# Kernel optimization log

Hardware: AMD Instinct MI355X
Metric: run time of the kernel (lower is better)

The kernel has to match this reference:

```python
import jax, jax.numpy as jnp
import numpy as np


def _pairwise_l2(x, y):
    # x: [N, D], y: [M, D] -> [N, M] Euclidean distances, computed via the
    # intermediate the original torch code materializes).
    x2 = jnp.sum(x * x, axis=-1)                      # [N]
    y2 = jnp.sum(y * y, axis=-1)                      # [M]
    xy = x @ y.T                                      # [N, M]
    d2 = jnp.maximum(x2[:, None] + y2[None, :] - 2.0 * xy, 0.0)
    return jnp.sqrt(d2)


def setup_inputs() -> dict:
    key = jax.random.key(0)
    k1, k2 = jax.random.split(key)
    pred = jax.random.normal(k1, (8192, 3), dtype=jnp.float32)
    label = jax.random.normal(k2, (8192, 3), dtype=jnp.float32)
    return {"pred": pred, "label": label}


def reference(pred, label):
    dis = _pairwise_l2(pred, label)                   # [N, M]
    dis_xy = jnp.mean(jnp.min(dis, axis=1))           # mean over x of nearest y
    dis_yx = jnp.mean(jnp.min(dis, axis=0))           # mean over y of nearest x
    return dis_xy + dis_yx
```

## Files before the change

kernel.cpp:

```cpp
#include <hip/hip_runtime.h>

constexpr int N    = 8192;
constexpr int BLK  = 256;
constexpr int BX   = 128;
constexpr int BY   = 2048;
constexpr int NYR  = N / BY;
constexpr int P    = 8;
constexpr int NSL  = 16;
constexpr int SY   = BY / NSL;
constexpr int SPAD = SY + 1;
constexpr int RPAD = BX + 4;

__global__ __launch_bounds__(BLK) void chamfer_stage1(
    const float* __restrict__ pred, const float* __restrict__ label,
    float* __restrict__ minbuf)
{
    int b   = blockIdx.x;
    int dir = b >> 8;
    int xbk = (b >> 2) & 63;
    int yr  = b & 3;

    const float* A = dir ? label : pred;
    const float* B = dir ? pred  : label;

    __shared__ float4 sy[NSL * SPAD];
    __shared__ float  red[NSL * RPAD];

    int u  = threadIdx.x & 15;
    int ys = threadIdx.x >> 4;

    float xa[P], xb[P], xc[P], nx[P], m[P];
    #pragma unroll
    for (int k = 0; k < P; ++k) {
        int idx = xbk * BX + k * 16 + u;
        float a = A[3*idx], c = A[3*idx+1], d = A[3*idx+2];
        xa[k] = -2.f * a;  xb[k] = -2.f * c;  xc[k] = -2.f * d;
        nx[k] = a*a + c*c + d*d;
        m[k]  = 3.4e38f;
    }

    for (int i = threadIdx.x; i < BY; i += BLK) {
        int g = yr * BY + i;
        float a = B[3*g], c = B[3*g+1], d = B[3*g+2];
        sy[(i >> 7) * SPAD + (i & (SY-1))] = make_float4(a, c, d, a*a + c*c + d*d);
    }
    __syncthreads();

    const float4* s = &sy[ys * SPAD];
    #pragma unroll 4
    for (int j = 0; j < SY; j += 2) {
        float4 ya = s[j], yb = s[j + 1];
        #pragma unroll
        for (int k = 0; k < P; ++k) {
            float sa = fmaf(xa[k], ya.x, fmaf(xb[k], ya.y, fmaf(xc[k], ya.z, ya.w)));
            float sb = fmaf(xa[k], yb.x, fmaf(xb[k], yb.y, fmaf(xc[k], yb.z, yb.w)));
            m[k] = fminf(fminf(sa, sb), m[k]);
        }
    }

    #pragma unroll
    for (int k = 0; k < P; ++k)
        red[ys * RPAD + k * 16 + u] = fmaxf(m[k] + nx[k], 0.f);
    __syncthreads();

    if (threadIdx.x < BX) {
        float v = red[threadIdx.x];
        #pragma unroll
        for (int q = 1; q < NSL; ++q)
            v = fminf(v, red[q * RPAD + threadIdx.x]);
        minbuf[yr * (2 * N) + dir * N + xbk * BX + threadIdx.x] = v;
    }
}

__global__ __launch_bounds__(256) void chamfer_stage2(
    const float4* __restrict__ minbuf4, float* __restrict__ bsum)
{
    int g = blockIdx.x * 256 + threadIdx.x;
    float4 v = minbuf4[g];
    #pragma unroll
    for (int r = 1; r < NYR; ++r) {
        float4 w = minbuf4[r * 4096 + g];
        v.x = fminf(v.x, w.x); v.y = fminf(v.y, w.y);
        v.z = fminf(v.z, w.z); v.w = fminf(v.w, w.w);
    }
    float s = sqrtf(v.x) + sqrtf(v.y) + sqrtf(v.z) + sqrtf(v.w);
    for (int off = 32; off; off >>= 1) s += __shfl_down(s, off);
    __shared__ float r2[4];
    if ((threadIdx.x & 63) == 0) r2[threadIdx.x >> 6] = s;
    __syncthreads();
    if (threadIdx.x == 0)
        bsum[blockIdx.x] = r2[0] + r2[1] + r2[2] + r2[3];
}

__global__ __launch_bounds__(64) void chamfer_stage3(
    const float* __restrict__ bsum, float* __restrict__ out)
{
    float s = (threadIdx.x < 16) ? bsum[threadIdx.x] : 0.f;
    for (int off = 32; off; off >>= 1) s += __shfl_down(s, off);
    if (threadIdx.x == 0) out[0] = s * (1.0f / N);
}

extern "C" void kernel_launch(void* const* d_in, const int* in_sizes, int n_in,
                              void* d_out, int out_size, void* d_ws, size_t ws_size,
                              hipStream_t stream) {
    const float* pred  = (const float*)d_in[0];
    const float* label = (const float*)d_in[1];
    float* out    = (float*)d_out;
    float* minbuf = (float*)d_ws;
    float* bsum   = minbuf + NYR * 2 * N;

    chamfer_stage1<<<dim3(2 * (N / BX) * NYR), dim3(BLK), 0, stream>>>(pred, label, minbuf);
    chamfer_stage2<<<dim3(16), dim3(256), 0, stream>>>((const float4*)minbuf, bsum);
    chamfer_stage3<<<dim3(1), dim3(64), 0, stream>>>(bsum, out);
}
```

Baseline: 19.69 us.

## Fuse final reduction into stage2 via last-block atomic counter; prefetch LDS loads

Removes the third kernel launch. Stage2 blocks atomically increment a counter reset by stage1, and the last block to finish sums the 16 partial sums and writes the output. The stage1 inner loop now software-pipelines its shared-memory loads, fetching the next pair of points while the current pair is computed, and the unroll factor goes from 4 to 8. This saves one launch gap at the cost of a fence, an atomic and higher register pressure.

```diff
diff --git a/kernel.cpp b/kernel.cpp
--- a/kernel.cpp
+++ b/kernel.cpp
@@ -13,8 +13,11 @@
 
 __global__ __launch_bounds__(BLK) void chamfer_stage1(
     const float* __restrict__ pred, const float* __restrict__ label,
-    float* __restrict__ minbuf)
+    float* __restrict__ minbuf, unsigned int* __restrict__ counter)
 {
+    if (blockIdx.x == 0 && threadIdx.x == 0)
+        __hip_atomic_store(counter, 0u, __ATOMIC_RELAXED, __HIP_MEMORY_SCOPE_AGENT);
+
     int b   = blockIdx.x;
     int dir = b >> 8;
     int xbk = (b >> 2) & 63;
@@ -29,13 +32,13 @@
     int u  = threadIdx.x & 15;
     int ys = threadIdx.x >> 4;
 
-    float xa[P], xb[P], xc[P], nx[P], m[P];
+    float cxa[P], cxb[P], cxc[P], xn[P], m[P];
     #pragma unroll
     for (int k = 0; k < P; ++k) {
         int idx = xbk * BX + k * 16 + u;
         float a = A[3*idx], c = A[3*idx+1], d = A[3*idx+2];
-        xa[k] = -2.f * a;  xb[k] = -2.f * c;  xc[k] = -2.f * d;
-        nx[k] = a*a + c*c + d*d;
+        cxa[k] = -2.f * a;  cxb[k] = -2.f * c;  cxc[k] = -2.f * d;
+        xn[k] = a*a + c*c + d*d;
         m[k]  = 3.4e38f;
     }
 
@@ -47,20 +50,28 @@
     __syncthreads();
 
     const float4* s = &sy[ys * SPAD];
-    #pragma unroll 4
-    for (int j = 0; j < SY; j += 2) {
-        float4 ya = s[j], yb = s[j + 1];
+    float4 y0 = s[0], y1 = s[1];
+    #pragma unroll 8
+    for (int j = 0; j < SY - 2; j += 2) {
+        float4 t0 = s[j + 2], t1 = s[j + 3];
         #pragma unroll
         for (int k = 0; k < P; ++k) {
-            float sa = fmaf(xa[k], ya.x, fmaf(xb[k], ya.y, fmaf(xc[k], ya.z, ya.w)));
-            float sb = fmaf(xa[k], yb.x, fmaf(xb[k], yb.y, fmaf(xc[k], yb.z, yb.w)));
+            float sa = fmaf(cxa[k], y0.x, fmaf(cxb[k], y0.y, fmaf(cxc[k], y0.z, y0.w)));
+            float sb = fmaf(cxa[k], y1.x, fmaf(cxb[k], y1.y, fmaf(cxc[k], y1.z, y1.w)));
             m[k] = fminf(fminf(sa, sb), m[k]);
         }
+        y0 = t0; y1 = t1;
+    }
+    #pragma unroll
+    for (int k = 0; k < P; ++k) {
+        float sa = fmaf(cxa[k], y0.x, fmaf(cxb[k], y0.y, fmaf(cxc[k], y0.z, y0.w)));
+        float sb = fmaf(cxa[k], y1.x, fmaf(cxb[k], y1.y, fmaf(cxc[k], y1.z, y1.w)));
+        m[k] = fminf(fminf(sa, sb), m[k]);
     }
 
     #pragma unroll
     for (int k = 0; k < P; ++k)
-        red[ys * RPAD + k * 16 + u] = fmaxf(m[k] + nx[k], 0.f);
+        red[ys * RPAD + k * 16 + u] = fmaxf(m[k] + xn[k], 0.f);
     __syncthreads();
 
     if (threadIdx.x < BX) {
@@ -73,7 +84,8 @@
 }
 
 __global__ __launch_bounds__(256) void chamfer_stage2(
-    const float4* __restrict__ minbuf4, float* __restrict__ bsum)
+    const float4* __restrict__ minbuf4, float* __restrict__ bsum,
+    unsigned int* __restrict__ counter, float* __restrict__ out)
 {
     int g = blockIdx.x * 256 + threadIdx.x;
     float4 v = minbuf4[g];
@@ -86,18 +98,27 @@
     float s = sqrtf(v.x) + sqrtf(v.y) + sqrtf(v.z) + sqrtf(v.w);
     for (int off = 32; off; off >>= 1) s += __shfl_down(s, off);
     __shared__ float r2[4];
+    __shared__ unsigned int isLast;
     if ((threadIdx.x & 63) == 0) r2[threadIdx.x >> 6] = s;
     __syncthreads();
-    if (threadIdx.x == 0)
+    if (threadIdx.x == 0) {
         bsum[blockIdx.x] = r2[0] + r2[1] + r2[2] + r2[3];
-}
+        __threadfence();
+        unsigned int old = atomicAdd(counter, 1u);
+        isLast = (old == 15u) ? 1u : 0u;
+    }
+    __syncthreads();
+    if (!isLast) return;
 
-__global__ __launch_bounds__(64) void chamfer_stage3(
-    const float* __restrict__ bsum, float* __restrict__ out)
-{
-    float s = (threadIdx.x < 16) ? bsum[threadIdx.x] : 0.f;
-    for (int off = 32; off; off >>= 1) s += __shfl_down(s, off);
-    if (threadIdx.x == 0) out[0] = s * (1.0f / N);
+    __threadfence();
+    if (threadIdx.x < 64) {
+        float t = (threadIdx.x < 16)
+            ? __hip_atomic_load(&bsum[threadIdx.x], __ATOMIC_RELAXED,
+                                __HIP_MEMORY_SCOPE_AGENT)
+            : 0.f;
+        for (int off = 8; off; off >>= 1) t += __shfl_down(t, off, 64);
+        if (threadIdx.x == 0) out[0] = t * (1.0f / N);
+    }
 }
 
 extern "C" void kernel_launch(void* const* d_in, const int* in_sizes, int n_in,
@@ -108,8 +129,8 @@
     float* out    = (float*)d_out;
     float* minbuf = (float*)d_ws;
     float* bsum   = minbuf + NYR * 2 * N;
+    unsigned int* counter = (unsigned int*)(bsum + 16);
 
-    chamfer_stage1<<<dim3(2 * (N / BX) * NYR), dim3(BLK), 0, stream>>>(pred, label, minbuf);
-    chamfer_stage2<<<dim3(16), dim3(256), 0, stream>>>((const float4*)minbuf, bsum);
-    chamfer_stage3<<<dim3(1), dim3(64), 0, stream>>>(bsum, out);
+    chamfer_stage1<<<dim3(2 * (N / BX) * NYR), dim3(BLK), 0, stream>>>(pred, label, minbuf, counter);
+    chamfer_stage2<<<dim3(16), dim3(256), 0, stream>>>((const float4*)minbuf, bsum, counter, out);
 }
```

New measurement: 20.62 us. 1.05x slower.
